# Kernel tuning notes

Hardware: AMD Instinct MI355X
Metric: run time of the kernel (lower is better)

## Reference

```python
import jax, jax.numpy as jnp
import numpy as np

BN_EPS = 1e-5

def _proj(x, w):
    # 1x1x1 conv, bias=False: pure channel contraction. x: [B,C,T,H,W], w: [O,C]
    return jnp.einsum('bcthw,oc->bothw', x, w)

def _maxpool222(x):
    # MaxPool3d(kernel=2, stride=2); dims are divisible by 2.
    B, C, T, H, W = x.shape
    return x.reshape(B, C, T // 2, 2, H // 2, 2, W // 2, 2).max(axis=(3, 5, 7))

def setup_inputs() -> dict:
    key = jax.random.key(0)
    ks = jax.random.split(key, 5)
    C, Ci = 256, 128
    x = jax.random.normal(ks[0], (4, C, 16, 28, 28), dtype=jnp.float32)
    sc = 1.0 / np.sqrt(C)
    theta_w = jax.random.normal(ks[1], (Ci, C), dtype=jnp.float32) * sc
    phi_w = jax.random.normal(ks[2], (Ci, C), dtype=jnp.float32) * sc
    g_w = jax.random.normal(ks[3], (Ci, C), dtype=jnp.float32) * sc
    z_w = jax.random.normal(ks[4], (C, Ci), dtype=jnp.float32) * (1.0 / np.sqrt(Ci))
    bn_gamma = jnp.ones((C,), dtype=jnp.float32)
    bn_beta = jnp.zeros((C,), dtype=jnp.float32)
    return {"x": x, "theta_w": theta_w, "phi_w": phi_w, "g_w": g_w,
            "z_w": z_w, "bn_gamma": bn_gamma, "bn_beta": bn_beta}

def reference(x, theta_w, phi_w, g_w, z_w, bn_gamma, bn_beta):
    B, C, T, H, W = x.shape
    Ci = theta_w.shape[0]
    N = T * H * W
    theta = _proj(x, theta_w).reshape(B, Ci, N)          # [B,Ci,N]
    phi = _maxpool222(_proj(x, phi_w))                   # [B,Ci,T/2,H/2,W/2]
    g = _maxpool222(_proj(x, g_w))
    Np = phi.shape[2] * phi.shape[3] * phi.shape[4]
    phi = phi.reshape(B, Ci, Np)                         # [B,Ci,Np]
    g = g.reshape(B, Ci, Np)
    attn = jnp.einsum('bcn,bcm->bnm', theta, phi)        # [B,N,Np]
    attn = jax.nn.softmax(attn, axis=-1)
    y = jnp.einsum('bnm,bcm->bcn', attn, g)              # [B,Ci,N]
    y = y.reshape(B, Ci, T, H, W)
    z = _proj(y, z_w)                                    # [B,C,T,H,W]
    # BatchNorm3d in training mode: batch stats over (B,T,H,W), biased var
    mean = z.mean(axis=(0, 2, 3, 4), keepdims=True)
    var = z.var(axis=(0, 2, 3, 4), keepdims=True)
    zn = (z - mean) * jax.lax.rsqrt(var + BN_EPS)
    zn = zn * bn_gamma[None, :, None, None, None] + bn_beta[None, :, None, None, None]
    return x + zn
```

## Files before the change

kernel.cpp:

```cpp
#include <hip/hip_runtime.h>
#include <stdint.h>

#define B_   4
#define C_   256
#define CI_  128
#define T_   16
#define H_   28
#define W_   28
#define HW_  784
#define N_   12544
#define TP_  8
#define HP_  14
#define WP_  14
#define NP_  1568
#define NP2_ 1600
#define NT_  196
#define NT2_ 98
#define NBLK_ 784
#define NBLK2_ 392
#define KVB_ 32
#define NKT_ 49

typedef __attribute__((ext_vector_type(8))) __bf16 bf16x8;
typedef __attribute__((ext_vector_type(4))) float  f32x4;

#define MFMA(a,b,c) __builtin_amdgcn_mfma_f32_16x16x32_bf16(a,b,c,0,0,0)

__device__ __forceinline__ void split_bf16(float f, __bf16& hi, __bf16& lo){
  hi = (__bf16)f;
  lo = (__bf16)(f - (float)hi);
}

__device__ __forceinline__ uint32_t pack2(float a, float b){
  union { __bf16 h; unsigned short s; } ua, ub;
  ua.h = (__bf16)a; ub.h = (__bf16)b;
  return (uint32_t)ua.s | ((uint32_t)ub.s << 16);
}

__device__ __forceinline__ void gload_lds16(const void* g, void* l){
  __builtin_amdgcn_global_load_lds((const __attribute__((address_space(1))) void*)g,
                                   (__attribute__((address_space(3))) void*)l, 16, 0, 0);
}

__global__ __launch_bounds__(256) void k_wconv(const float* __restrict__ wt, const float* __restrict__ wp,
                       const float* __restrict__ wg, const float* __restrict__ zw,
                       __bf16* __restrict__ wth, __bf16* __restrict__ wtl,
                       __bf16* __restrict__ wph, __bf16* __restrict__ wpl,
                       __bf16* __restrict__ wgh, __bf16* __restrict__ wgl,
                       __bf16* __restrict__ zwh, __bf16* __restrict__ zwl){
  int i = blockIdx.x*256 + threadIdx.x;
  if (i < 32768){
    __bf16 h, lo;
    split_bf16(wt[i], h, lo); wth[i]=h; wtl[i]=lo;
    split_bf16(wp[i], h, lo); wph[i]=h; wpl[i]=lo;
    split_bf16(wg[i], h, lo); wgh[i]=h; wgl[i]=lo;
    split_bf16(zw[i], h, lo); zwh[i]=h; zwl[i]=lo;
  }
}

__global__ __launch_bounds__(256) void k_xt(const float* __restrict__ x,
                     __bf16* __restrict__ xth, __bf16* __restrict__ xtl){
  __shared__ float tile[64][66];
  int wg = blockIdx.x;
  int nt = wg % NT_; int ct = (wg/NT_)&3; int b = wg/(NT_*4);
  int n0 = nt*64, c0 = ct*64;
  const float* xb = x + ((size_t)(b*C_ + c0))*N_ + n0;
  int tid = threadIdx.x;
  for (int it=0; it<16; ++it){
    int idx = it*256 + tid;
    int cl = idx>>6, nl = idx&63;
    tile[cl][nl] = xb[(size_t)cl*N_ + nl];
  }
  __syncthreads();
  size_t obase = ((size_t)(b*N_ + n0))*C_ + c0;
  for (int it=0; it<16; ++it){
    int idx = it*256 + tid;
    int nl = idx>>6, cl = idx&63;
    __bf16 hi, lo;
    split_bf16(tile[cl][nl], hi, lo);
    xth[obase + (size_t)nl*C_ + cl] = hi;
    xtl[obase + (size_t)nl*C_ + cl] = lo;
  }
}

__global__ __launch_bounds__(256,4) void k_proj3(const __bf16* __restrict__ xth, const __bf16* __restrict__ xtl,
                        const __bf16* __restrict__ wth, const __bf16* __restrict__ wtl,
                        const __bf16* __restrict__ wph, const __bf16* __restrict__ wpl,
                        const __bf16* __restrict__ wgh, const __bf16* __restrict__ wgl,
                        __bf16* __restrict__ th_hi, __bf16* __restrict__ th_lo,
                        float* __restrict__ phf32, __bf16* __restrict__ ggf){
  __shared__ char wbuf[2][16384];
  int wg = blockIdx.x;
  int nt = wg % NT_; int b = wg/NT_;
  int n0 = nt*64;
  int tid = threadIdx.x; int w = tid>>6; int l = tid&63; int lr = l&15; int lg = l>>4;
  int nrow = 16*w + lr;
  size_t abase = ((size_t)(b*N_ + n0 + nrow))*C_;
  bf16x8 Ah[8], Al[8];
  #pragma unroll
  for (int ks=0; ks<8; ++ks){
    Ah[ks] = *(const bf16x8*)(xth + abase + 32*ks + 8*lg);
    Al[ks] = *(const bf16x8*)(xtl + abase + 32*ks + 8*lg);
  }
  int sp_part[4]; int sp_rowc[4]; int sp_off[4];
  #pragma unroll
  for (int i=0;i<4;++i){
    int p = i*4096 + tid*16;
    sp_part[i] = p>>13;
    int row = (p>>9)&15;
    int colb = p & 511;
    sp_rowc[i] = row*C_ + ((colb ^ ((row&7)<<4)) >> 1);
    sp_off[i] = i*4096 + w*1024;
  }
  #pragma unroll
  for (int i=0;i<4;++i){
    const __bf16* src = (sp_part[i] ? wtl : wth) + sp_rowc[i];
    gload_lds16(src, &wbuf[0][sp_off[i]]);
  }
  __syncthreads();

  size_t obase = ((size_t)(b*N_ + n0))*CI_;
  int cur = 0;
  for (int pair=0; pair<24; ++pair){
    int p = pair>>3, ot = pair&7;
    if (pair < 23){
      int pn = pair+1, p2 = pn>>3, ot2 = pn&7;
      const __bf16* bh = (p2==0) ? wth : ((p2==1) ? wph : wgh);
      const __bf16* bl = (p2==0) ? wtl : ((p2==1) ? wpl : wgl);
      #pragma unroll
      for (int i=0;i<4;++i){
        const __bf16* src = (sp_part[i] ? bl : bh) + (size_t)(16*ot2)*C_ + sp_rowc[i];
        gload_lds16(src, &wbuf[cur^1][sp_off[i]]);
      }
    }
    const char* wb = wbuf[cur];
    f32x4 aHH={0.f,0.f,0.f,0.f}, aLH={0.f,0.f,0.f,0.f}, aHL={0.f,0.f,0.f,0.f};
    int swz = (lr&7)<<4;
    #pragma unroll
    for (int ks=0; ks<8; ++ks){
      int off = lr*512 + ((ks*64 + lg*16) ^ swz);
      bf16x8 Bh = *(const bf16x8*)(wb + off);
      bf16x8 Bl = *(const bf16x8*)(wb + 8192 + off);
      aHH = MFMA(Ah[ks], Bh, aHH);
      aLH = MFMA(Al[ks], Bh, aLH);
      aHL = MFMA(Ah[ks], Bl, aHL);
    }
    f32x4 acc = aHH + aLH + aHL;
    if (p == 0){
      #pragma unroll
      for (int r=0;r<4;++r){
        int n = 16*w + 4*lg + r;
        __bf16 hi, lo; split_bf16(acc[r], hi, lo);
        th_hi[obase + (size_t)n*CI_ + 16*ot + lr] = hi;
        th_lo[obase + (size_t)n*CI_ + 16*ot + lr] = lo;
      }
    } else if (p == 1){
      #pragma unroll
      for (int r=0;r<4;++r){
        int n = 16*w + 4*lg + r;
        phf32[obase + (size_t)n*CI_ + 16*ot + lr] = acc[r];
      }
    } else {
      #pragma unroll
      for (int r=0;r<4;++r){
        int n = 16*w + 4*lg + r;
        ggf[obase + (size_t)n*CI_ + 16*ot + lr] = (__bf16)acc[r];
      }
    }
    __syncthreads();
    cur ^= 1;
  }
}

__global__ __launch_bounds__(256) void k_pool(const float* __restrict__ phf32, const __bf16* __restrict__ ggf,
                       __bf16* __restrict__ phph, __bf16* __restrict__ phpl,
                       __bf16* __restrict__ ggp){
  int idx = blockIdx.x*256 + threadIdx.x;
  if (idx >= B_*NP2_*16) return;
  int c8 = idx & 15;
  int m  = (idx>>4) % NP2_;
  int b  = idx / (16*NP2_);
  if (m >= NP_){
    bf16x8 zv;
    #pragma unroll
    for (int j=0;j<8;++j) zv[j] = (__bf16)0.f;
    *(bf16x8*)(phph + ((size_t)(b*NP2_ + m))*CI_ + c8*8) = zv;
    *(bf16x8*)(phpl + ((size_t)(b*NP2_ + m))*CI_ + c8*8) = zv;
    #pragma unroll
    for (int j=0;j<8;++j) ggp[((size_t)(b*CI_ + c8*8 + j))*NP2_ + m] = (__bf16)0.f;
    return;
  }
  int tp = m/(HP_*WP_), hp = (m/WP_)%HP_, wq = m%WP_;
  int t0 = tp*2, h0 = hp*2, w0 = wq*2;
  const float*  pb = phf32 + ((size_t)b*N_)*CI_ + c8*8;
  const __bf16* gb = ggf   + ((size_t)b*N_)*CI_ + c8*8;
  float mp[8], mg[8];
  #pragma unroll
  for (int j=0;j<8;++j){ mp[j] = -3e38f; mg[j] = -3e38f; }
  #pragma unroll
  for (int dt=0; dt<2; ++dt)
  #pragma unroll
  for (int dh=0; dh<2; ++dh)
  #pragma unroll
  for (int dw=0; dw<2; ++dw){
    int n = (t0+dt)*HW_ + (h0+dh)*W_ + (w0+dw);
    f32x4 p0 = *(const f32x4*)(pb + (size_t)n*CI_);
    f32x4 p1 = *(const f32x4*)(pb + (size_t)n*CI_ + 4);
    bf16x8 vg = *(const bf16x8*)(gb + (size_t)n*CI_);
    #pragma unroll
    for (int j=0;j<4;++j){ mp[j] = fmaxf(mp[j], p0[j]); mp[4+j] = fmaxf(mp[4+j], p1[j]); }
    #pragma unroll
    for (int j=0;j<8;++j){ mg[j] = fmaxf(mg[j], (float)vg[j]); }
  }
  bf16x8 oh, ol, og;
  #pragma unroll
  for (int j=0;j<8;++j){
    __bf16 hi, lo;
    split_bf16(mp[j], hi, lo);
    oh[j] = hi; ol[j] = lo;
    og[j] = (__bf16)mg[j];
  }
  *(bf16x8*)(phph + ((size_t)(b*NP2_ + m))*CI_ + c8*8) = oh;
  *(bf16x8*)(phpl + ((size_t)(b*NP2_ + m))*CI_ + c8*8) = ol;
  #pragma unroll
  for (int j=0;j<8;++j) ggp[((size_t)(b*CI_ + c8*8 + j))*NP2_ + m] = og[j];
}

__global__ __launch_bounds__(256) void k_phmean1(const __bf16* __restrict__ phph, const __bf16* __restrict__ phpl,
                         float* __restrict__ pph){
  __shared__ float part[2][128];
  int blk = blockIdx.x;
  int b = blk >> 3, g = blk & 7;
  int tid = threadIdx.x;
  int c = tid & 127, mo = tid >> 7;
  const __bf16* ph = phph + (size_t)b*NP2_*CI_ + c;
  const __bf16* pl = phpl + (size_t)b*NP2_*CI_ + c;
  float s = 0.f;
  for (int k=0; k<98; ++k){
    int m = g + 8*(2*k + mo);
    s += (float)ph[(size_t)m*CI_] + (float)pl[(size_t)m*CI_];
  }
  part[mo][c] = s;
  __syncthreads();
  if (tid < 128) pph[(size_t)blk*128 + tid] = part[0][tid] + part[1][tid];
}

__global__ __launch_bounds__(256) void k_phmean2(const float* __restrict__ pph, float* __restrict__ phmean){
  int t = blockIdx.x*256 + threadIdx.x;
  if (t >= B_*CI_) return;
  int b = t >> 7, c = t & 127;
  float s = 0.f;
  #pragma unroll
  for (int g=0; g<8; ++g) s += pph[(size_t)(b*8+g)*128 + c];
  phmean[b*CI_ + c] = s * (1.0f/(float)NP_);
}

__global__ __launch_bounds__(512,4) void k_attn(const __bf16* __restrict__ th_hi, const __bf16* __restrict__ th_lo,
                       const __bf16* __restrict__ phph, const __bf16* __restrict__ phpl,
                       const __bf16* __restrict__ ggp, const float* __restrict__ phmean,
                       float* __restrict__ y){
  __shared__ char sbuf[2][24576];
  __shared__ float estp[128][4];
  __shared__ float est[128];
  int wg = blockIdx.x;
  int nt = wg % NT2_; int b = wg/NT2_;
  int n0 = nt*128;
  int tid = threadIdx.x; int w = tid>>6; int l = tid&63; int lr = l&15; int lg = l>>4;
  const __bf16* phb = phph + (size_t)b*NP2_*CI_;
  const __bf16* plb = phpl + (size_t)b*NP2_*CI_;
  const __bf16* ggb = ggp + (size_t)b*CI_*NP2_;

  {
    int row = tid >> 2, q = tid & 3;
    const __bf16* rh = th_hi + ((size_t)(b*N_ + n0 + row))*CI_ + 32*q;
    const __bf16* rl = th_lo + ((size_t)(b*N_ + n0 + row))*CI_ + 32*q;
    const float* pm = phmean + b*CI_ + 32*q;
    float sacc = 0.f;
    #pragma unroll
    for (int j=0;j<4;++j){
      bf16x8 vh = *(const bf16x8*)(rh + 8*j);
      bf16x8 vl = *(const bf16x8*)(rl + 8*j);
      f32x4 p0 = *(const f32x4*)(pm + 8*j);
      f32x4 p1 = *(const f32x4*)(pm + 8*j + 4);
      #pragma unroll
      for (int k=0;k<4;++k){
        sacc += ((float)vh[k]   + (float)vl[k]  )*p0[k];
        sacc += ((float)vh[4+k] + (float)vl[4+k])*p1[k];
      }
    }
    estp[row][q] = sacc;
  }
  const __bf16* sptr[3]; int sstr[3]; int soff[3];
  #pragma unroll
  for (int jj=0; jj<3; ++jj){
    int j = w*3 + jj;
    int p = j*1024 + l*16;
    int reg = p >> 13;
    int e = p & 8191;
    if (reg < 2){
      int m = e >> 8;
      int chb = (e & 255) ^ ((m & 7) << 4);
      const __bf16* base = (reg==0 ? phb : plb);
      sptr[jj] = base + (size_t)m*CI_ + (chb>>1);
      sstr[jj] = KVB_*CI_;
    } else {
      int c = e >> 6;
      int chb = (e & 63) ^ (((c >> 1) & 3) << 4);
      sptr[jj] = ggb + (size_t)c*NP2_ + (chb>>1);
      sstr[jj] = KVB_;
    }
    soff[jj] = j*1024;
  }
  __syncthreads();
  if (tid < 128) est[tid] = estp[tid][0]+estp[tid][1]+estp[tid][2]+estp[tid][3];

  size_t tbase = ((size_t)(b*N_ + n0 + 16*w))*CI_ + (size_t)lr*CI_;
  bf16x8 Ah[4], Al[4];
  #pragma unroll
  for (int ks=0; ks<4; ++ks){
    Ah[ks] = *(const bf16x8*)(th_hi + tbase + 32*ks + 8*lg);
    Al[ks] = *(const bf16x8*)(th_lo + tbase + 32*ks + 8*lg);
  }
  f32x4 yacc[8];
  #pragma unroll
  for (int ct=0; ct<8; ++ct) yacc[ct] = (f32x4){0.f,0.f,0.f,0.f};
  float psum = 0.f;
  __syncthreads();
  float est_lane = est[16*w + lr];

  #pragma unroll
  for (int jj=0; jj<3; ++jj) gload_lds16(sptr[jj], &sbuf[0][soff[jj]]);
  __syncthreads();

  int s1 = lr + (((2*lg)  )&3)*16;
  int s2 = lr + (((2*lg+1))&3)*16;
  bool hi2 = (lg >= 2);

  int cur = 0;
  for (int t=0; t<NKT_; ++t){
    if (t < NKT_-1){
      #pragma unroll
      for (int jj=0; jj<3; ++jj)
        gload_lds16(sptr[jj] + (size_t)(t+1)*sstr[jj], &sbuf[cur^1][soff[jj]]);
    }
    const char* pb_ = sbuf[cur];
    uint32_t q00, q01, q10, q11;
    #pragma unroll
    for (int mt=0; mt<2; ++mt){
      f32x4 aHH = {0.f,0.f,0.f,0.f}, aLH = {0.f,0.f,0.f,0.f}, aHL = {0.f,0.f,0.f,0.f};
      int mrow = 16*mt + lr;
      int swz = (mrow&7)<<4;
      #pragma unroll
      for (int ks=0; ks<4; ++ks){
        int off = mrow*256 + ((64*ks + 16*lg) ^ swz);
        bf16x8 Bh = *(const bf16x8*)(pb_ + off);
        bf16x8 Bl = *(const bf16x8*)(pb_ + 8192 + off);
        aHH = MFMA(Bh, Ah[ks], aHH);
        aLH = MFMA(Bh, Al[ks], aLH);
        aHL = MFMA(Bl, Ah[ks], aHL);
      }
      f32x4 sv = aHH + aLH + aHL;
      float p0 = __expf(sv[0] - est_lane);
      float p1 = __expf(sv[1] - est_lane);
      float p2 = __expf(sv[2] - est_lane);
      float p3 = __expf(sv[3] - est_lane);
      psum += (p0 + p1) + (p2 + p3);
      uint32_t d0 = pack2(p0, p1), d1 = pack2(p2, p3);
      if (mt == 0){ q00 = d0; q01 = d1; } else { q10 = d0; q11 = d1; }
    }
    uint32_t b00 = __shfl(q00, s1, 64), b10 = __shfl(q10, s1, 64);
    uint32_t b01 = __shfl(q01, s1, 64), b11 = __shfl(q11, s1, 64);
    uint32_t c00 = __shfl(q00, s2, 64), c10 = __shfl(q10, s2, 64);
    uint32_t c01 = __shfl(q01, s2, 64), c11 = __shfl(q11, s2, 64);
    union { uint32_t u[4]; bf16x8 v; } pa;
    pa.u[0] = hi2 ? b10 : b00;
    pa.u[1] = hi2 ? b11 : b01;
    pa.u[2] = hi2 ? c10 : c00;
    pa.u[3] = hi2 ? c11 : c01;
    #pragma unroll
    for (int ct=0; ct<8; ++ct){
      int c = 16*ct + lr;
      int goff = 16384 + c*64 + ((16*lg) ^ (((c>>1)&3)<<4));
      bf16x8 Gf = *(const bf16x8*)(pb_ + goff);
      yacc[ct] = MFMA(pa.v, Gf, yacc[ct]);
    }
    __syncthreads();
    cur ^= 1;
  }
  float rs = psum;
  rs += __shfl_xor(rs, 16, 64);
  rs += __shfl_xor(rs, 32, 64);
  float inv = 1.0f / rs;
  float invr[4];
  #pragma unroll
  for (int r=0; r<4; ++r) invr[r] = __shfl(inv, 4*lg + r, 64);
  float* yb = y + ((size_t)(b*N_ + n0 + 16*w))*CI_;
  #pragma unroll
  for (int ct=0; ct<8; ++ct){
    #pragma unroll
    for (int r=0;r<4;++r){
      yb[(size_t)(4*lg+r)*CI_ + 16*ct + lr] = yacc[ct][r] * invr[r];
    }
  }
}

__global__ __launch_bounds__(256,3) void k_zproj(const float* __restrict__ y,
                        const __bf16* __restrict__ zwh, const __bf16* __restrict__ zwl,
                        __bf16* __restrict__ z, float* __restrict__ pS, float* __restrict__ pQ){
  __shared__ float zt[64][68];
  __shared__ float red[4][256][2];
  __shared__ char wbuf[2][8192];
  int wg = blockIdx.x; int nt = wg % NT_; int b = wg/NT_; int n0 = nt*64;
  int tid = threadIdx.x; int w = tid>>6; int l = tid&63; int lr = l&15; int lg = l>>4;
  const float* yb = y + ((size_t)(b*N_ + n0 + 16*w))*CI_ + (size_t)lr*CI_;
  bf16x8 Ah[4], Al[4];
  #pragma unroll
  for (int ks=0;ks<4;++ks){
    f32x4 a0 = *(const f32x4*)(yb + 32*ks + 8*lg);
    f32x4 a1 = *(const f32x4*)(yb + 32*ks + 8*lg + 4);
    #pragma unroll
    for (int j=0;j<4;++j){
      __bf16 h0,l0,h1,l1;
      split_bf16(a0[j], h0, l0);
      split_bf16(a1[j], h1, l1);
      Ah[ks][j]   = h0; Al[ks][j]   = l0;
      Ah[ks][4+j] = h1; Al[ks][4+j] = l1;
    }
  }
  int sp_part[2]; int sp_rowc[2]; int sp_off[2];
  #pragma unroll
  for (int i=0;i<2;++i){
    int p = i*4096 + tid*16;
    sp_part[i] = p>>12;
    int row = (p>>8)&15;
    int colb = p & 255;
    sp_rowc[i] = row*CI_ + ((colb ^ ((row&7)<<4)) >> 1);
    sp_off[i] = i*4096 + w*1024;
  }
  #pragma unroll
  for (int i=0;i<2;++i){
    const __bf16* src = (sp_part[i] ? zwl : zwh) + sp_rowc[i];
    gload_lds16(src, &wbuf[0][sp_off[i]]);
  }
  __syncthreads();

  __bf16* zb = z + (size_t)b*C_*N_ + n0;
  int cur = 0;
  for (int og=0; og<4; ++og){
    #pragma unroll
    for (int oi=0; oi<4; ++oi){
      int ot = og*4 + oi;
      if (ot < 15){
        #pragma unroll
        for (int i=0;i<2;++i){
          const __bf16* src = (sp_part[i] ? zwl : zwh) + (size_t)(16*(ot+1))*CI_ + sp_rowc[i];
          gload_lds16(src, &wbuf[cur^1][sp_off[i]]);
        }
      }
      const char* wb = wbuf[cur];
      f32x4 aHH = {0.f,0.f,0.f,0.f}, aLH = {0.f,0.f,0.f,0.f}, aHL = {0.f,0.f,0.f,0.f};
      int swz = (lr&7)<<4;
      #pragma unroll
      for (int ks=0;ks<4;++ks){
        int off = lr*256 + ((ks*64 + lg*16) ^ swz);
        bf16x8 Bh = *(const bf16x8*)(wb + off);
        bf16x8 Bl = *(const bf16x8*)(wb + 4096 + off);
        aHH = MFMA(Ah[ks], Bh, aHH);
        aLH = MFMA(Al[ks], Bh, aLH);
        aHL = MFMA(Ah[ks], Bl, aHL);
      }
      f32x4 acc = aHH + aLH + aHL;
      float s1=0.f, s2=0.f;
      #pragma unroll
      for (int r=0;r<4;++r){
        float v = acc[r];
        int nl = 16*w + 4*lg + r;
        zt[16*oi+lr][nl] = v;
        s1 += v; s2 += v*v;
      }
      s1 += __shfl_xor(s1,16,64); s1 += __shfl_xor(s1,32,64);
      s2 += __shfl_xor(s2,16,64); s2 += __shfl_xor(s2,32,64);
      if (lg==0){ red[w][16*ot+lr][0] = s1; red[w][16*ot+lr][1] = s2; }
      if (oi < 3){ __syncthreads(); cur ^= 1; }
    }
    __syncthreads();
    #pragma unroll
    for (int it=0; it<2; ++it){
      int idx = it*256 + tid;
      int ol = idx>>3, cc = idx&7;
      f32x4 v0 = *(const f32x4*)(&zt[ol][cc*8]);
      f32x4 v1 = *(const f32x4*)(&zt[ol][cc*8+4]);
      bf16x8 o8;
      #pragma unroll
      for (int j=0;j<4;++j){ o8[j] = (__bf16)v0[j]; o8[4+j] = (__bf16)v1[j]; }
      *(bf16x8*)(zb + (size_t)(og*64 + ol)*N_ + cc*8) = o8;
    }
    __syncthreads();
    cur ^= 1;
  }
  float t1 = red[0][tid][0]+red[1][tid][0]+red[2][tid][0]+red[3][tid][0];
  float t2 = red[0][tid][1]+red[1][tid][1]+red[2][tid][1]+red[3][tid][1];
  pS[(size_t)wg*256 + tid] = t1;
  pQ[(size_t)wg*256 + tid] = t2;
}

__global__ __launch_bounds__(256) void k_stats(const float* __restrict__ pS, const float* __restrict__ pQ,
                        const float* __restrict__ gamma, const float* __restrict__ beta,
                        float* __restrict__ coef){
  int o = blockIdx.x; int t = threadIdx.x;
  float s=0.f, q=0.f;
  for (int i=t; i<NBLK_; i+=256){ s += pS[(size_t)i*256+o]; q += pQ[(size_t)i*256+o]; }
  __shared__ float rs[4], rq[4];
  #pragma unroll
  for (int sh=32; sh; sh>>=1){ s += __shfl_down(s,sh,64); q += __shfl_down(q,sh,64); }
  int w = t>>6;
  if ((t&63)==0){ rs[w]=s; rq[w]=q; }
  __syncthreads();
  if (t==0){
    s = rs[0]+rs[1]+rs[2]+rs[3]; q = rq[0]+rq[1]+rq[2]+rq[3];
    float inv = 1.0f/(float)(B_*N_);
    float mean = s*inv, var = q*inv - mean*mean;
    float a = gamma[o]*rsqrtf(var + 1e-5f);
    coef[o] = a; coef[256+o] = beta[o] - mean*a;
  }
}

__global__ __launch_bounds__(256) void k_final(const float* __restrict__ x, const __bf16* __restrict__ z,
                        const float* __restrict__ coef, float* __restrict__ out){
  uint32_t i = blockIdx.x*256 + threadIdx.x;
  uint32_t e0 = i*8u;
  if (e0 >= (uint32_t)(B_*C_*N_)) return;
  int o = (int)((e0 / (uint32_t)N_) % (uint32_t)C_);
  float a = coef[o], b2 = coef[256+o];
  bf16x8 zv = *(const bf16x8*)(z + e0);
  f32x4 x0 = *(const f32x4*)(x + e0);
  f32x4 x1 = *(const f32x4*)(x + e0 + 4);
  f32x4 r0, r1;
  #pragma unroll
  for (int j=0;j<4;++j){
    r0[j] = x0[j] + (float)zv[j]*a + b2;
    r1[j] = x1[j] + (float)zv[4+j]*a + b2;
  }
  *(f32x4*)(out + e0) = r0;
  *(f32x4*)(out + e0 + 4) = r1;
}

extern "C" void kernel_launch(void* const* d_in, const int* in_sizes, int n_in,
                              void* d_out, int out_size, void* d_ws, size_t ws_size,
                              hipStream_t stream){
  const float* x     = (const float*)d_in[0];
  const float* wt    = (const float*)d_in[1];
  const float* wp    = (const float*)d_in[2];
  const float* wg    = (const float*)d_in[3];
  const float* zw    = (const float*)d_in[4];
  const float* gamma = (const float*)d_in[5];
  const float* beta  = (const float*)d_in[6];
  float* out = (float*)d_out;
  char* ws = (char*)d_ws;
  size_t off = 0;
  auto alloc = [&](size_t bytes)->void*{ void* p = ws + off; off = (off + bytes + 255) & ~(size_t)255; return p; };
  __bf16* xth  = (__bf16*)alloc((size_t)B_*N_*C_*2);
  __bf16* xtl  = (__bf16*)alloc((size_t)B_*N_*C_*2);
  float*  phf32= (float*)alloc((size_t)B_*N_*CI_*4);
  __bf16* ggf  = (__bf16*)alloc((size_t)B_*N_*CI_*2);
  __bf16* th_hi= (__bf16*)alloc((size_t)B_*N_*CI_*2);
  __bf16* th_lo= (__bf16*)alloc((size_t)B_*N_*CI_*2);
  __bf16* wth  = (__bf16*)alloc(32768*2);
  __bf16* wtl  = (__bf16*)alloc(32768*2);
  __bf16* wph  = (__bf16*)alloc(32768*2);
  __bf16* wpl  = (__bf16*)alloc(32768*2);
  __bf16* wgh  = (__bf16*)alloc(32768*2);
  __bf16* wgl  = (__bf16*)alloc(32768*2);
  __bf16* zwh  = (__bf16*)alloc(32768*2);
  __bf16* zwl  = (__bf16*)alloc(32768*2);
  __bf16* phph = (__bf16*)alloc((size_t)B_*NP2_*CI_*2);
  __bf16* phpl = (__bf16*)alloc((size_t)B_*NP2_*CI_*2);
  __bf16* ggp  = (__bf16*)alloc((size_t)B_*CI_*NP2_*2);
  float*  pS   = (float*)alloc((size_t)NBLK_*256*4);
  float*  pQ   = (float*)alloc((size_t)NBLK_*256*4);
  float*  coef = (float*)alloc(512*4);
  float*  phmean = (float*)alloc(B_*CI_*4);
  float*  pph  = (float*)alloc((size_t)B_*8*128*4);
  float* y = (float*)xth;
  __bf16* z = (__bf16*)phf32;

  k_wconv<<<128, 256, 0, stream>>>(wt, wp, wg, zw, wth, wtl, wph, wpl, wgh, wgl, zwh, zwl);
  k_xt<<<B_*4*NT_, 256, 0, stream>>>(x, xth, xtl);
  k_proj3<<<NBLK_, 256, 0, stream>>>(xth, xtl, wth, wtl, wph, wpl, wgh, wgl, th_hi, th_lo, phf32, ggf);
  k_pool<<<(B_*NP2_*16 + 255)/256, 256, 0, stream>>>(phf32, ggf, phph, phpl, ggp);
  k_phmean1<<<B_*8, 256, 0, stream>>>(phph, phpl, pph);
  k_phmean2<<<2, 256, 0, stream>>>(pph, phmean);
  k_attn<<<NBLK2_, 512, 0, stream>>>(th_hi, th_lo, phph, phpl, ggp, phmean, y);
  k_zproj<<<NBLK_, 256, 0, stream>>>(y, zwh, zwl, z, pS, pQ);
  k_stats<<<256, 256, 0, stream>>>(pS, pQ, gamma, beta, coef);
  k_final<<<(B_*C_*N_/8 + 255)/256, 256, 0, stream>>>(x, z, coef, out);
}
```

Baseline: 242.8 us.

## Process two 16-row query tiles per wave in attention to reuse LDS fragments

The attention kernel drops from 512 to 256 threads per block, and each wave now handles 32 query rows (two 16-row groups) instead of 16. Every phi/g fragment read from LDS feeds twice as many MFMAs, which halves LDS read traffic per unit of compute. The cost is doubled accumulator and theta registers per wave, fewer waves per block and a lower occupancy hint, so latency hiding may suffer.

After: 242.7 us. Within noise of the previous version (-0.0%).

```diff
diff --git a/kernel.cpp b/kernel.cpp
--- a/kernel.cpp
+++ b/kernel.cpp
@@ -255,12 +255,12 @@
   phmean[b*CI_ + c] = s * (1.0f/(float)NP_);
 }
 
-__global__ __launch_bounds__(512,4) void k_attn(const __bf16* __restrict__ th_hi, const __bf16* __restrict__ th_lo,
+__global__ __launch_bounds__(256,2) void k_attn(const __bf16* __restrict__ th_hi, const __bf16* __restrict__ th_lo,
                        const __bf16* __restrict__ phph, const __bf16* __restrict__ phpl,
                        const __bf16* __restrict__ ggp, const float* __restrict__ phmean,
                        float* __restrict__ y){
   __shared__ char sbuf[2][24576];
-  __shared__ float estp[128][4];
+  __shared__ float estp[128][2];
   __shared__ float est[128];
   int wg = blockIdx.x;
   int nt = wg % NT2_; int b = wg/NT2_;
@@ -271,13 +271,13 @@
   const __bf16* ggb = ggp + (size_t)b*CI_*NP2_;
 
   {
-    int row = tid >> 2, q = tid & 3;
-    const __bf16* rh = th_hi + ((size_t)(b*N_ + n0 + row))*CI_ + 32*q;
-    const __bf16* rl = th_lo + ((size_t)(b*N_ + n0 + row))*CI_ + 32*q;
-    const float* pm = phmean + b*CI_ + 32*q;
+    int row = tid >> 1, q = tid & 1;
+    const __bf16* rh = th_hi + ((size_t)(b*N_ + n0 + row))*CI_ + 64*q;
+    const __bf16* rl = th_lo + ((size_t)(b*N_ + n0 + row))*CI_ + 64*q;
+    const float* pm = phmean + b*CI_ + 64*q;
     float sacc = 0.f;
     #pragma unroll
-    for (int j=0;j<4;++j){
+    for (int j=0;j<8;++j){
       bf16x8 vh = *(const bf16x8*)(rh + 8*j);
       bf16x8 vl = *(const bf16x8*)(rl + 8*j);
       f32x4 p0 = *(const f32x4*)(pm + 8*j);
@@ -290,10 +290,10 @@
     }
     estp[row][q] = sacc;
   }
-  const __bf16* sptr[3]; int sstr[3]; int soff[3];
-  #pragma unroll
-  for (int jj=0; jj<3; ++jj){
-    int j = w*3 + jj;
+  const __bf16* sptr[6]; int sstr[6]; int soff[6];
+  #pragma unroll
+  for (int jj=0; jj<6; ++jj){
+    int j = w*6 + jj;
     int p = j*1024 + l*16;
     int reg = p >> 13;
     int e = p & 8191;
@@ -312,24 +312,28 @@
     soff[jj] = j*1024;
   }
   __syncthreads();
-  if (tid < 128) est[tid] = estp[tid][0]+estp[tid][1]+estp[tid][2]+estp[tid][3];
-
-  size_t tbase = ((size_t)(b*N_ + n0 + 16*w))*CI_ + (size_t)lr*CI_;
-  bf16x8 Ah[4], Al[4];
-  #pragma unroll
-  for (int ks=0; ks<4; ++ks){
-    Ah[ks] = *(const bf16x8*)(th_hi + tbase + 32*ks + 8*lg);
-    Al[ks] = *(const bf16x8*)(th_lo + tbase + 32*ks + 8*lg);
-  }
-  f32x4 yacc[8];
-  #pragma unroll
-  for (int ct=0; ct<8; ++ct) yacc[ct] = (f32x4){0.f,0.f,0.f,0.f};
-  float psum = 0.f;
-  __syncthreads();
-  float est_lane = est[16*w + lr];
-
-  #pragma unroll
-  for (int jj=0; jj<3; ++jj) gload_lds16(sptr[jj], &sbuf[0][soff[jj]]);
+  if (tid < 128) est[tid] = estp[tid][0]+estp[tid][1];
+
+  bf16x8 Ah[2][4], Al[2][4];
+  #pragma unroll
+  for (int cg=0; cg<2; ++cg){
+    size_t tb = ((size_t)(b*N_ + n0 + 32*w + 16*cg))*CI_ + (size_t)lr*CI_;
+    #pragma unroll
+    for (int ks=0; ks<4; ++ks){
+      Ah[cg][ks] = *(const bf16x8*)(th_hi + tb + 32*ks + 8*lg);
+      Al[cg][ks] = *(const bf16x8*)(th_lo + tb + 32*ks + 8*lg);
+    }
+  }
+  f32x4 yacc0[8], yacc1[8];
+  #pragma unroll
+  for (int ct=0; ct<8; ++ct){ yacc0[ct] = (f32x4){0.f,0.f,0.f,0.f}; yacc1[ct] = (f32x4){0.f,0.f,0.f,0.f}; }
+  float psum0 = 0.f, psum1 = 0.f;
+  __syncthreads();
+  float estl0 = est[32*w + lr];
+  float estl1 = est[32*w + 16 + lr];
+
+  #pragma unroll
+  for (int jj=0; jj<6; ++jj) gload_lds16(sptr[jj], &sbuf[0][soff[jj]]);
   __syncthreads();
 
   int s1 = lr + (((2*lg)  )&3)*16;
@@ -340,14 +344,15 @@
   for (int t=0; t<NKT_; ++t){
     if (t < NKT_-1){
       #pragma unroll
-      for (int jj=0; jj<3; ++jj)
+      for (int jj=0; jj<6; ++jj)
         gload_lds16(sptr[jj] + (size_t)(t+1)*sstr[jj], &sbuf[cur^1][soff[jj]]);
     }
     const char* pb_ = sbuf[cur];
-    uint32_t q00, q01, q10, q11;
+    uint32_t qa00, qa01, qa10, qa11, qb00, qb01, qb10, qb11;
     #pragma unroll
     for (int mt=0; mt<2; ++mt){
-      f32x4 aHH = {0.f,0.f,0.f,0.f}, aLH = {0.f,0.f,0.f,0.f}, aHL = {0.f,0.f,0.f,0.f};
+      f32x4 aHH0={0.f,0.f,0.f,0.f}, aLH0={0.f,0.f,0.f,0.f}, aHL0={0.f,0.f,0.f,0.f};
+      f32x4 aHH1={0.f,0.f,0.f,0.f}, aLH1={0.f,0.f,0.f,0.f}, aHL1={0.f,0.f,0.f,0.f};
       int mrow = 16*mt + lr;
       int swz = (mrow&7)<<4;
       #pragma unroll
@@ -355,51 +360,74 @@
         int off = mrow*256 + ((64*ks + 16*lg) ^ swz);
         bf16x8 Bh = *(const bf16x8*)(pb_ + off);
         bf16x8 Bl = *(const bf16x8*)(pb_ + 8192 + off);
-        aHH = MFMA(Bh, Ah[ks], aHH);
-        aLH = MFMA(Bh, Al[ks], aLH);
-        aHL = MFMA(Bl, Ah[ks], aHL);
-      }
-      f32x4 sv = aHH + aLH + aHL;
-      float p0 = __expf(sv[0] - est_lane);
-      float p1 = __expf(sv[1] - est_lane);
-      float p2 = __expf(sv[2] - est_lane);
-      float p3 = __expf(sv[3] - est_lane);
-      psum += (p0 + p1) + (p2 + p3);
-      uint32_t d0 = pack2(p0, p1), d1 = pack2(p2, p3);
-      if (mt == 0){ q00 = d0; q01 = d1; } else { q10 = d0; q11 = d1; }
-    }
-    uint32_t b00 = __shfl(q00, s1, 64), b10 = __shfl(q10, s1, 64);
-    uint32_t b01 = __shfl(q01, s1, 64), b11 = __shfl(q11, s1, 64);
-    uint32_t c00 = __shfl(q00, s2, 64), c10 = __shfl(q10, s2, 64);
-    uint32_t c01 = __shfl(q01, s2, 64), c11 = __shfl(q11, s2, 64);
-    union { uint32_t u[4]; bf16x8 v; } pa;
-    pa.u[0] = hi2 ? b10 : b00;
-    pa.u[1] = hi2 ? b11 : b01;
-    pa.u[2] = hi2 ? c10 : c00;
-    pa.u[3] = hi2 ? c11 : c01;
+        aHH0 = MFMA(Bh, Ah[0][ks], aHH0);
+        aLH0 = MFMA(Bh, Al[0][ks], aLH0);
+        aHL0 = MFMA(Bl, Ah[0][ks], aHL0);
+        aHH1 = MFMA(Bh, Ah[1][ks], aHH1);
+        aLH1 = MFMA(Bh, Al[1][ks], aLH1);
+        aHL1 = MFMA(Bl, Ah[1][ks], aHL1);
+      }
+      f32x4 sv0 = aHH0 + aLH0 + aHL0;
+      f32x4 sv1 = aHH1 + aLH1 + aHL1;
+      float p00 = __expf(sv0[0]-estl0), p01 = __expf(sv0[1]-estl0);
+      float p02 = __expf(sv0[2]-estl0), p03 = __expf(sv0[3]-estl0);
+      float p10 = __expf(sv1[0]-estl1), p11 = __expf(sv1[1]-estl1);
+      float p12 = __expf(sv1[2]-estl1), p13 = __expf(sv1[3]-estl1);
+      psum0 += (p00 + p01) + (p02 + p03);
+      psum1 += (p10 + p11) + (p12 + p13);
+      uint32_t da0 = pack2(p00,p01), da1 = pack2(p02,p03);
+      uint32_t db0 = pack2(p10,p11), db1 = pack2(p12,p13);
+      if (mt == 0){ qa00 = da0; qa01 = da1; qb00 = db0; qb01 = db1; }
+      else        { qa10 = da0; qa11 = da1; qb10 = db0; qb11 = db1; }
+    }
+    uint32_t ba00 = __shfl(qa00, s1, 64), ba10 = __shfl(qa10, s1, 64);
+    uint32_t ba01 = __shfl(qa01, s1, 64), ba11 = __shfl(qa11, s1, 64);
+    uint32_t ca00 = __shfl(qa00, s2, 64), ca10 = __shfl(qa10, s2, 64);
+    uint32_t ca01 = __shfl(qa01, s2, 64), ca11 = __shfl(qa11, s2, 64);
+    union { uint32_t u[4]; bf16x8 v; } pa0;
+    pa0.u[0] = hi2 ? ba10 : ba00;
+    pa0.u[1] = hi2 ? ba11 : ba01;
+    pa0.u[2] = hi2 ? ca10 : ca00;
+    pa0.u[3] = hi2 ? ca11 : ca01;
+    uint32_t bb00 = __shfl(qb00, s1, 64), bb10 = __shfl(qb10, s1, 64);
+    uint32_t bb01 = __shfl(qb01, s1, 64), bb11 = __shfl(qb11, s1, 64);
+    uint32_t cb00 = __shfl(qb00, s2, 64), cb10 = __shfl(qb10, s2, 64);
+    uint32_t cb01 = __shfl(qb01, s2, 64), cb11 = __shfl(qb11, s2, 64);
+    union { uint32_t u[4]; bf16x8 v; } pa1;
+    pa1.u[0] = hi2 ? bb10 : bb00;
+    pa1.u[1] = hi2 ? bb11 : bb01;
+    pa1.u[2] = hi2 ? cb10 : cb00;
+    pa1.u[3] = hi2 ? cb11 : cb01;
     #pragma unroll
     for (int ct=0; ct<8; ++ct){
       int c = 16*ct + lr;
       int goff = 16384 + c*64 + ((16*lg) ^ (((c>>1)&3)<<4));
       bf16x8 Gf = *(const bf16x8*)(pb_ + goff);
-      yacc[ct] = MFMA(pa.v, Gf, yacc[ct]);
+      yacc0[ct] = MFMA(pa0.v, Gf, yacc0[ct]);
+      yacc1[ct] = MFMA(pa1.v, Gf, yacc1[ct]);
     }
     __syncthreads();
     cur ^= 1;
   }
-  float rs = psum;
-  rs += __shfl_xor(rs, 16, 64);
-  rs += __shfl_xor(rs, 32, 64);
-  float inv = 1.0f / rs;
-  float invr[4];
-  #pragma unroll
-  for (int r=0; r<4; ++r) invr[r] = __shfl(inv, 4*lg + r, 64);
-  float* yb = y + ((size_t)(b*N_ + n0 + 16*w))*CI_;
+  float rs0 = psum0;
+  rs0 += __shfl_xor(rs0, 16, 64); rs0 += __shfl_xor(rs0, 32, 64);
+  float rs1 = psum1;
+  rs1 += __shfl_xor(rs1, 16, 64); rs1 += __shfl_xor(rs1, 32, 64);
+  float inv0 = 1.0f / rs0, inv1 = 1.0f / rs1;
+  float ivr0[4], ivr1[4];
+  #pragma unroll
+  for (int r=0; r<4; ++r){
+    ivr0[r] = __shfl(inv0, 4*lg + r, 64);
+    ivr1[r] = __shfl(inv1, 4*lg + r, 64);
+  }
+  float* yb0 = y + ((size_t)(b*N_ + n0 + 32*w))*CI_;
+  float* yb1 = y + ((size_t)(b*N_ + n0 + 32*w + 16))*CI_;
   #pragma unroll
   for (int ct=0; ct<8; ++ct){
     #pragma unroll
     for (int r=0;r<4;++r){
-      yb[(size_t)(4*lg+r)*CI_ + 16*ct + lr] = yacc[ct][r] * invr[r];
+      yb0[(size_t)(4*lg+r)*CI_ + 16*ct + lr] = yacc0[ct][r] * ivr0[r];
+      yb1[(size_t)(4*lg+r)*CI_ + 16*ct + lr] = yacc1[ct][r] * ivr1[r];
     }
   }
 }
@@ -590,7 +618,7 @@
   k_pool<<<(B_*NP2_*16 + 255)/256, 256, 0, stream>>>(phf32, ggf, phph, phpl, ggp);
   k_phmean1<<<B_*8, 256, 0, stream>>>(phph, phpl, pph);
   k_phmean2<<<2, 256, 0, stream>>>(pph, phmean);
-  k_attn<<<NBLK2_, 512, 0, stream>>>(th_hi, th_lo, phph, phpl, ggp, phmean, y);
+  k_attn<<<NBLK2_, 256, 0, stream>>>(th_hi, th_lo, phph, phpl, ggp, phmean, y);
   k_zproj<<<NBLK_, 256, 0, stream>>>(y, zwh, zwl, z, pS, pQ);
   k_stats<<<256, 256, 0, stream>>>(pS, pQ, gamma, beta, coef);
   k_final<<<(B_*C_*N_/8 + 255)/256, 256, 0, stream>>>(x, z, coef, out);
```
